# Kernel optimization log

Measured on AMD Instinct MI355X. Metric: run time of the kernel, lower is better.

Reference implementation:

```python
import jax, jax.numpy as jnp
import numpy as np

N = 100000   # nodes
E = 1600000  # edges
F_IN = 64    # n_features
H = 32       # hidden_size
OUT = 1      # output_size


def _lin(k, fan_in, fan_out):
    return (jax.random.normal(k, (fan_in, fan_out), jnp.float32) / np.sqrt(fan_in)).astype(jnp.float32)


def setup_inputs() -> dict:
    key = jax.random.key(0)
    ks = jax.random.split(key, 16)
    x = jax.random.normal(ks[0], (N, F_IN), jnp.float32)
    edge_index = jax.random.randint(ks[1], (2, E), 0, N, dtype=jnp.int64)
    # guarantee current_node (=0) has outgoing edges so the legal-move mask is non-empty
    edge_index = edge_index.at[0, :64].set(0)
    edge_attr = jax.random.uniform(ks[2], (E,), jnp.float32)
    return {
        "x": x, "edge_index": edge_index, "edge_attr": edge_attr, "current_node": 0,
        # conv_in: GraphConv(F_IN -> H)
        "Win_rel": _lin(ks[3], F_IN, H), "bin_rel": jnp.zeros((H,), jnp.float32), "Win_root": _lin(ks[4], F_IN, H),
        # conv_hidden: GraphConv(H -> H)
        "Wh_rel": _lin(ks[5], H, H), "bh_rel": jnp.zeros((H,), jnp.float32), "Wh_root": _lin(ks[6], H, H),
        # policy_conv: GraphConv(H -> OUT)
        "Wp_rel": _lin(ks[7], H, OUT), "bp_rel": jnp.zeros((OUT,), jnp.float32), "Wp_root": _lin(ks[8], H, OUT),
        # value_conv: GraphConv(H -> OUT)
        "Wv_rel": _lin(ks[9], H, OUT), "bv_rel": jnp.zeros((OUT,), jnp.float32), "Wv_root": _lin(ks[10], H, OUT),
    }


def _graph_conv(h, src, dst, ew, W_rel, b_rel, W_root):
    # PyG GraphConv: out_i = W_root h_i + W_rel * sum_{j->i} e_ji * h_j + b
    msg = h[src] * ew[:, None]                              # [E, d] gather + scale
    agg = jax.ops.segment_sum(msg, dst, num_segments=N)      # [N, d] scatter-add
    return agg @ W_rel + b_rel + h @ W_root


def reference(x, edge_index, edge_attr, current_node,
              Win_rel, bin_rel, Win_root,
              Wh_rel, bh_rel, Wh_root,
              Wp_rel, bp_rel, Wp_root,
              Wv_rel, bv_rel, Wv_root):
    src, dst = edge_index[0], edge_index[1]
    h = jax.nn.relu(_graph_conv(x, src, dst, edge_attr, Win_rel, bin_rel, Win_root))
    h = jax.nn.relu(_graph_conv(h, src, dst, edge_attr, Wh_rel, bh_rel, Wh_root))
    p = _graph_conv(h, src, dst, edge_attr, Wp_rel, bp_rel, Wp_root)  # [N, 1]
    v = _graph_conv(h, src, dst, edge_attr, Wv_rel, bv_rel, Wv_root)  # [N, 1]
    # illegal_moves_mask: 1 for nodes directly reachable from current_node
    hit = (src == current_node).astype(jnp.float32)
    mask = (jnp.zeros((N,), jnp.float32).at[dst].add(hit) > 0).astype(jnp.float32)
    p_m = mask * p.T                                   # [1, N]
    p_m = jnp.where(p_m == 0, -jnp.inf, p_m)
    p_soft = jax.nn.softmax(p_m, axis=1)
    v_m = mask * v.T                                   # [1, N]
    return p_soft.reshape(-1), v_m.reshape(-1)
```

## Files before the change

kernel.cpp:

```cpp
#include <hip/hip_runtime.h>
#include <hip/hip_fp16.h>
#include <cmath>

static constexpr int NN = 100000;
static constexpr int NE = 1600000;
static const size_t NW = (size_t)NN * 32;
static constexpr int SUB = 256;
static constexpr int NSUB = 391;
static constexpr int CH = 8192;
static constexpr int NCH = (NE + CH - 1) / CH;
static constexpr int BCAP = 5200;
static constexpr int CSRN = NSUB * BCAP;
static constexpr int MCAP = 4096;

__device__ __forceinline__ float ent_w(unsigned e)
{
    return __half2float(__ushort_as_half((unsigned short)(e >> 17)));
}
__device__ __forceinline__ int ent_s(unsigned e)
{
    int s = (int)(e & 0x1FFFF);
    return s < NN ? s : NN - 1;
}

__device__ __forceinline__ float4 pack8(const float* v)
{
    union { __half2 h2[4]; float4 f4; } u;
    u.h2[0] = __floats2half2_rn(v[0], v[1]);
    u.h2[1] = __floats2half2_rn(v[2], v[3]);
    u.h2[2] = __floats2half2_rn(v[4], v[5]);
    u.h2[3] = __floats2half2_rn(v[6], v[7]);
    return u.f4;
}

__global__ void __launch_bounds__(512) fused_build_mm1_k(
    const int* __restrict__ src, const int* __restrict__ dst,
    const float* __restrict__ ew, const int* __restrict__ curp,
    int* __restrict__ maskb, int* __restrict__ mcount, int* __restrict__ mlist,
    int* __restrict__ bcnt, unsigned* __restrict__ bx,
    unsigned char* __restrict__ bd,
    const float* __restrict__ x, const float* __restrict__ Wrel,
    const float* __restrict__ Wroot, const float* __restrict__ bin,
    __half* __restrict__ proj1, __half* __restrict__ root1)
{
    __shared__ union {
        struct {
            unsigned sBufX[CH];
            unsigned char sBufD[CH];
            int lhist[NSUB];
            int lpos[NSUB];
            int lstart[NSUB];
            int lbase[NSUB];
            int tscan[512];
        } s;
        struct {
            float sX[128 * 65];
            float sW[64 * 68];
        } m;
    } u;

    int t = threadIdx.x;
    int bid = blockIdx.x;

    if (bid < NCH) {
        for (int i = t; i < NSUB; i += 512) { u.s.lhist[i] = 0; u.s.lpos[i] = 0; }
        __syncthreads();
        int c0 = bid * CH;
        int cur = curp[0];
        unsigned rx[CH / 512];
        int rd[CH / 512];
#pragma unroll
        for (int it = 0; it < CH / 512; ++it) {
            int e = c0 + it * 512 + t;
            rd[it] = -1;
            if (e < NE) {
                int d = dst[e];
                int sv = src[e];
                if ((unsigned)d < (unsigned)NN) {
                    rd[it] = d;
                    unsigned bits = __half_as_ushort(__float2half(ew[e]));
                    rx[it] = ((unsigned)sv & 0x1FFFF) | (bits << 17);
                    atomicAdd(&u.s.lhist[d >> 8], 1);
                    if (sv == cur) {
                        if (atomicExch(maskb + d, 1) == 0) {
                            int idx = atomicAdd(mcount, 1);
                            if (idx < MCAP) mlist[idx] = d;
                        }
                    }
                }
            }
        }
        __syncthreads();
        int v = (t < NSUB) ? u.s.lhist[t] : 0;
        u.s.tscan[t] = v;
        __syncthreads();
        for (int sh = 1; sh < 512; sh <<= 1) {
            int xv = u.s.tscan[t];
            int a = (t >= sh) ? u.s.tscan[t - sh] : 0;
            __syncthreads();
            u.s.tscan[t] = xv + a;
            __syncthreads();
        }
        if (t < NSUB) {
            u.s.lstart[t] = u.s.tscan[t] - v;
            u.s.lbase[t] = (v > 0) ? atomicAdd(&bcnt[t], v) : 0;
        }
        __syncthreads();
#pragma unroll
        for (int it = 0; it < CH / 512; ++it) {
            if (rd[it] >= 0) {
                int b = rd[it] >> 8;
                int p = atomicAdd(&u.s.lpos[b], 1);
                int pos = u.s.lstart[b] + p;
                u.s.sBufX[pos] = rx[it];
                u.s.sBufD[pos] = (unsigned char)(rd[it] & 255);
            }
        }
        __syncthreads();
        int grp = t >> 4, l16 = t & 15;
        for (int b = grp; b < NSUB; b += 32) {
            int s0 = u.s.lstart[b];
            int cb = u.s.lhist[b];
            int gb = u.s.lbase[b];
            size_t gb0 = (size_t)b * BCAP;
            for (int j = l16; j < cb; j += 16) {
                unsigned pos = (unsigned)(gb + j);
                if (pos < (unsigned)BCAP) {
                    bx[gb0 + pos] = u.s.sBufX[s0 + j];
                    bd[gb0 + pos] = u.s.sBufD[s0 + j];
                }
            }
        }
    } else {
        int mb = bid - NCH;
        for (int i = t; i < 64 * 32; i += 512) {
            int k = i >> 5, j = i & 31;
            u.m.sW[k * 68 + j] = Wrel[i];
            u.m.sW[k * 68 + 32 + j] = Wroot[i];
        }
        int base = mb * 128;
        for (int i = t; i < 2048; i += 512) {
            int node = i >> 4;
            int k = (i & 15) * 4;
            int n = base + node;
            if (n >= NN) n = NN - 1;
            float4 v4 = *(const float4*)(x + (size_t)n * 64 + k);
            float* p = u.m.sX + node * 65 + k;
            p[0] = v4.x; p[1] = v4.y; p[2] = v4.z; p[3] = v4.w;
        }
        __syncthreads();
        int cg = t & 7;
        int ng = t >> 3;
        int c0m = 8 * cg;
        float acc[2][8] = {};
        for (int k = 0; k < 64; ++k) {
            float xv0 = u.m.sX[(2 * ng + 0) * 65 + k];
            float xv1 = u.m.sX[(2 * ng + 1) * 65 + k];
            float4 w0 = *(const float4*)(u.m.sW + k * 68 + c0m);
            float4 w1 = *(const float4*)(u.m.sW + k * 68 + c0m + 4);
            const float* wp = (const float*)&w0;
#pragma unroll
            for (int j = 0; j < 4; ++j) {
                float w = wp[j];
                acc[0][j] = fmaf(xv0, w, acc[0][j]);
                acc[1][j] = fmaf(xv1, w, acc[1][j]);
            }
            const float* wq = (const float*)&w1;
#pragma unroll
            for (int j = 0; j < 4; ++j) {
                float w = wq[j];
                acc[0][4 + j] = fmaf(xv0, w, acc[0][4 + j]);
                acc[1][4 + j] = fmaf(xv1, w, acc[1][4 + j]);
            }
        }
#pragma unroll
        for (int r = 0; r < 2; ++r) {
            int n = base + 2 * ng + r;
            if (n >= NN) break;
            if (cg < 4) {
                *(float4*)(proj1 + (size_t)n * 32 + c0m) = pack8(acc[r]);
            } else {
                int c = c0m - 32;
                float vv[8];
#pragma unroll
                for (int j = 0; j < 8; ++j) vv[j] = acc[r][j] + bin[c + j];
                *(float4*)(root1 + (size_t)n * 32 + c) = pack8(vv);
            }
        }
    }
}

__global__ void __launch_bounds__(512) sortB_k(
    const unsigned* __restrict__ bx, const unsigned char* __restrict__ bd,
    const int* __restrict__ bcnt,
    unsigned* __restrict__ csr4, int* __restrict__ deg, int* __restrict__ off)
{
    __shared__ unsigned sX[BCAP];
    __shared__ unsigned char sD[BCAP];
    __shared__ int lhist[SUB];
    __shared__ int lstart[SUB];
    __shared__ int lcur[SUB];
    __shared__ int tscan[256];
    int g = blockIdx.x, t = threadIdx.x;
    if (t < SUB) { lhist[t] = 0; lcur[t] = 0; }
    __syncthreads();
    int cnt = bcnt[g];
    if (cnt < 0) cnt = 0;
    if (cnt > BCAP) cnt = BCAP;
    size_t gbase = (size_t)g * BCAP;
    for (int i = t; i < cnt; i += 512) {
        unsigned e = bx[gbase + i];
        unsigned char d = bd[gbase + i];
        sX[i] = e;
        sD[i] = d;
        atomicAdd(&lhist[d], 1);
    }
    __syncthreads();
    if (t < 256) tscan[t] = lhist[t];
    __syncthreads();
    for (int s = 1; s < 256; s <<= 1) {
        int x = 0, a = 0;
        if (t < 256) { x = tscan[t]; a = (t >= s) ? tscan[t - s] : 0; }
        __syncthreads();
        if (t < 256) tscan[t] = x + a;
        __syncthreads();
    }
    if (t < 256) lstart[t] = tscan[t] - lhist[t];
    __syncthreads();
    int base = g * BCAP;
    for (int i = t; i < cnt; i += 512) {
        int ld = (int)sD[i];
        int p = atomicAdd(&lcur[ld], 1);
        unsigned pos = (unsigned)(base + lstart[ld] + p);
        if (pos < (unsigned)CSRN) csr4[pos] = sX[i];
    }
    if (t < SUB) {
        int n = g * SUB + t;
        if (n < NN) {
            deg[n] = lhist[t];
            off[n] = base + lstart[t];
        }
    }
}

__global__ void __launch_bounds__(256) mm2_k(
    const __half* __restrict__ h1, const float* __restrict__ Wrel,
    const float* __restrict__ Wroot, const float* __restrict__ bh,
    __half* __restrict__ proj2, __half* __restrict__ root2)
{
    __shared__ float sX[128 * 33];
    __shared__ float sW[32 * 68];
    int t = threadIdx.x;
    for (int i = t; i < 32 * 32; i += 256) {
        int k = i >> 5, j = i & 31;
        sW[k * 68 + j] = Wrel[i];
        sW[k * 68 + 32 + j] = Wroot[i];
    }
    int base = blockIdx.x * 128;
    for (int i = t; i < 512; i += 256) {
        int node = i >> 2;
        int hs = (i & 3) * 8;
        int n = base + node;
        if (n >= NN) n = NN - 1;
        float4 v = *(const float4*)(h1 + (size_t)n * 32 + hs);
        const __half2* hp = (const __half2*)&v;
        float* p = sX + node * 33 + hs;
#pragma unroll
        for (int u = 0; u < 4; ++u) {
            float2 f2 = __half22float2(hp[u]);
            p[2 * u] = f2.x;
            p[2 * u + 1] = f2.y;
        }
    }
    __syncthreads();
    int cg = t & 7;
    int ng = t >> 3;
    int c0 = 8 * cg;
    float acc[4][8] = {};
    for (int k = 0; k < 32; ++k) {
        float xv0 = sX[(4 * ng + 0) * 33 + k];
        float xv1 = sX[(4 * ng + 1) * 33 + k];
        float xv2 = sX[(4 * ng + 2) * 33 + k];
        float xv3 = sX[(4 * ng + 3) * 33 + k];
        float4 w0 = *(const float4*)(sW + k * 68 + c0);
        float4 w1 = *(const float4*)(sW + k * 68 + c0 + 4);
        const float* wp = (const float*)&w0;
#pragma unroll
        for (int j = 0; j < 4; ++j) {
            float w = wp[j];
            acc[0][j] = fmaf(xv0, w, acc[0][j]);
            acc[1][j] = fmaf(xv1, w, acc[1][j]);
            acc[2][j] = fmaf(xv2, w, acc[2][j]);
            acc[3][j] = fmaf(xv3, w, acc[3][j]);
        }
        const float* wq = (const float*)&w1;
#pragma unroll
        for (int j = 0; j < 4; ++j) {
            float w = wq[j];
            acc[0][4 + j] = fmaf(xv0, w, acc[0][4 + j]);
            acc[1][4 + j] = fmaf(xv1, w, acc[1][4 + j]);
            acc[2][4 + j] = fmaf(xv2, w, acc[2][4 + j]);
            acc[3][4 + j] = fmaf(xv3, w, acc[3][4 + j]);
        }
    }
#pragma unroll
    for (int r = 0; r < 4; ++r) {
        int n = base + 4 * ng + r;
        if (n >= NN) break;
        if (cg < 4) {
            *(float4*)(proj2 + (size_t)n * 32 + c0) = pack8(acc[r]);
        } else {
            int c = c0 - 32;
            float v[8];
#pragma unroll
            for (int j = 0; j < 8; ++j) v[j] = acc[r][j] + bh[c + j];
            *(float4*)(root2 + (size_t)n * 32 + c) = pack8(v);
        }
    }
}

__global__ void __launch_bounds__(256) agg1_v4(
    const __half* __restrict__ proj1, const __half* __restrict__ root1,
    const unsigned* __restrict__ csr4, const int* __restrict__ off,
    const int* __restrict__ deg, __half* __restrict__ h1)
{
    int t = threadIdx.x;
    int q = t & 3;
    int f0 = q * 8;
    int n = blockIdx.x * 64 + (t >> 2);
    if (n >= NN) return;
    int st = off[n];
    int dg = deg[n];
    if (st < 0) st = 0;
    if (st > CSRN) st = CSRN;
    if (dg < 0) dg = 0;
    if (dg > CSRN - st) dg = CSRN - st;
    float acc[8] = {0.f, 0.f, 0.f, 0.f, 0.f, 0.f, 0.f, 0.f};
    int i = 0;
    for (; i + 1 < dg; i += 2) {
        unsigned e0 = csr4[st + i];
        unsigned e1 = csr4[st + i + 1];
        float w0 = ent_w(e0), w1 = ent_w(e1);
        float4 r0 = *(const float4*)(proj1 + (size_t)ent_s(e0) * 32 + f0);
        float4 r1 = *(const float4*)(proj1 + (size_t)ent_s(e1) * 32 + f0);
        const __half2* h0 = (const __half2*)&r0;
        const __half2* h1p = (const __half2*)&r1;
#pragma unroll
        for (int u = 0; u < 4; ++u) {
            float2 a = __half22float2(h0[u]);
            float2 b = __half22float2(h1p[u]);
            acc[2 * u] = fmaf(w0, a.x, acc[2 * u]);
            acc[2 * u + 1] = fmaf(w0, a.y, acc[2 * u + 1]);
            acc[2 * u] = fmaf(w1, b.x, acc[2 * u]);
            acc[2 * u + 1] = fmaf(w1, b.y, acc[2 * u + 1]);
        }
    }
    if (i < dg) {
        unsigned e0 = csr4[st + i];
        float w0 = ent_w(e0);
        float4 r0 = *(const float4*)(proj1 + (size_t)ent_s(e0) * 32 + f0);
        const __half2* h0 = (const __half2*)&r0;
#pragma unroll
        for (int u = 0; u < 4; ++u) {
            float2 a = __half22float2(h0[u]);
            acc[2 * u] = fmaf(w0, a.x, acc[2 * u]);
            acc[2 * u + 1] = fmaf(w0, a.y, acc[2 * u + 1]);
        }
    }
    float4 rr = *(const float4*)(root1 + (size_t)n * 32 + f0);
    const __half2* rp = (const __half2*)&rr;
    float h[8];
#pragma unroll
    for (int u = 0; u < 4; ++u) {
        float2 f2 = __half22float2(rp[u]);
        h[2 * u] = fmaxf(acc[2 * u] + f2.x, 0.f);
        h[2 * u + 1] = fmaxf(acc[2 * u + 1] + f2.y, 0.f);
    }
    *(float4*)(h1 + (size_t)n * 32 + f0) = pack8(h);
}

__global__ void __launch_bounds__(256) agg2_v4(
    const __half* __restrict__ proj2, const __half* __restrict__ root2,
    const float* __restrict__ Wp_rel, const float* __restrict__ Wp_root,
    const float* __restrict__ bp, const float* __restrict__ Wv_rel,
    const float* __restrict__ Wv_root, const float* __restrict__ bv,
    const unsigned* __restrict__ csr4, const int* __restrict__ off,
    const int* __restrict__ deg, float2* __restrict__ pv,
    float* __restrict__ pbase, float* __restrict__ vbase,
    float* __restrict__ out_p, float* __restrict__ out_v)
{
    __shared__ float sHead[4 * 32];
    if (threadIdx.x < 32) {
        sHead[threadIdx.x] = Wp_rel[threadIdx.x];
        sHead[32 + threadIdx.x] = Wp_root[threadIdx.x];
        sHead[64 + threadIdx.x] = Wv_rel[threadIdx.x];
        sHead[96 + threadIdx.x] = Wv_root[threadIdx.x];
    }
    __syncthreads();
    int t = threadIdx.x;
    int q = t & 3;
    int f0 = q * 8;
    int n = blockIdx.x * 64 + (t >> 2);
    if (n >= NN) return;
    int st = off[n];
    int dg = deg[n];
    if (st < 0) st = 0;
    if (st > CSRN) st = CSRN;
    if (dg < 0) dg = 0;
    if (dg > CSRN - st) dg = CSRN - st;
    float acc[8] = {0.f, 0.f, 0.f, 0.f, 0.f, 0.f, 0.f, 0.f};
    int i = 0;
    for (; i + 1 < dg; i += 2) {
        unsigned e0 = csr4[st + i];
        unsigned e1 = csr4[st + i + 1];
        float w0 = ent_w(e0), w1 = ent_w(e1);
        float4 r0 = *(const float4*)(proj2 + (size_t)ent_s(e0) * 32 + f0);
        float4 r1 = *(const float4*)(proj2 + (size_t)ent_s(e1) * 32 + f0);
        const __half2* h0 = (const __half2*)&r0;
        const __half2* h1p = (const __half2*)&r1;
#pragma unroll
        for (int u = 0; u < 4; ++u) {
            float2 a = __half22float2(h0[u]);
            float2 b = __half22float2(h1p[u]);
            acc[2 * u] = fmaf(w0, a.x, acc[2 * u]);
            acc[2 * u + 1] = fmaf(w0, a.y, acc[2 * u + 1]);
            acc[2 * u] = fmaf(w1, b.x, acc[2 * u]);
            acc[2 * u + 1] = fmaf(w1, b.y, acc[2 * u + 1]);
        }
    }
    if (i < dg) {
        unsigned e0 = csr4[st + i];
        float w0 = ent_w(e0);
        float4 r0 = *(const float4*)(proj2 + (size_t)ent_s(e0) * 32 + f0);
        const __half2* h0 = (const __half2*)&r0;
#pragma unroll
        for (int u = 0; u < 4; ++u) {
            float2 a = __half22float2(h0[u]);
            acc[2 * u] = fmaf(w0, a.x, acc[2 * u]);
            acc[2 * u + 1] = fmaf(w0, a.y, acc[2 * u + 1]);
        }
    }
    float4 rr = *(const float4*)(root2 + (size_t)n * 32 + f0);
    const __half2* rp = (const __half2*)&rr;
    float h[8];
#pragma unroll
    for (int u = 0; u < 4; ++u) {
        float2 f2 = __half22float2(rp[u]);
        h[2 * u] = fmaxf(acc[2 * u] + f2.x, 0.f);
        h[2 * u + 1] = fmaxf(acc[2 * u + 1] + f2.y, 0.f);
    }
    float prv = 0.f, pov = 0.f, vrv = 0.f, vov = 0.f;
#pragma unroll
    for (int j = 0; j < 8; ++j) {
        prv = fmaf(h[j], sHead[f0 + j], prv);
        pov = fmaf(h[j], sHead[32 + f0 + j], pov);
        vrv = fmaf(h[j], sHead[64 + f0 + j], vrv);
        vov = fmaf(h[j], sHead[96 + f0 + j], vov);
    }
#pragma unroll
    for (int m = 1; m <= 2; m <<= 1) {
        prv += __shfl_xor(prv, m, 64);
        pov += __shfl_xor(pov, m, 64);
        vrv += __shfl_xor(vrv, m, 64);
        vov += __shfl_xor(vov, m, 64);
    }
    if (q == 0) {
        pv[n] = make_float2(prv, vrv);
        pbase[n] = pov + bp[0];
        vbase[n] = vov + bv[0];
        out_p[n] = 0.f;
        out_v[n] = 0.f;
    }
}

__global__ void __launch_bounds__(256) masked_softmax_k(
    const int* __restrict__ mlist, const int* __restrict__ mcount,
    const unsigned* __restrict__ csr4, const int* __restrict__ off,
    const int* __restrict__ deg, const float2* __restrict__ pv,
    const float* __restrict__ pbase, const float* __restrict__ vbase,
    float* __restrict__ out_p, float* __restrict__ out_v)
{
    __shared__ float sPm[MCAP];
    __shared__ float sV[MCAP];
    __shared__ int sN[MCAP];
    __shared__ float sMx, sSum;
    __shared__ float sred[4];
    int m = mcount[0];
    if (m > MCAP) m = MCAP;
    if (m < 0) m = 0;
    for (int idx = threadIdx.x; idx < m; idx += 256) {
        int n = mlist[idx];
        if ((unsigned)n >= (unsigned)NN) n = 0;
        sN[idx] = n;
        int st = off[n];
        int dg = deg[n];
        if (st < 0) st = 0;
        if (st > CSRN) st = CSRN;
        if (dg < 0) dg = 0;
        if (dg > CSRN - st) dg = CSRN - st;
        float pa = 0.f, va = 0.f;
        for (int i = 0; i < dg; ++i) {
            unsigned ent = csr4[st + i];
            int s = ent_s(ent);
            float w = ent_w(ent);
            float2 tv = pv[s];
            pa = fmaf(tv.x, w, pa);
            va = fmaf(tv.y, w, va);
        }
        float p = pa + pbase[n];
        sPm[idx] = (p == 0.f) ? -INFINITY : p;
        sV[idx] = va + vbase[n];
    }
    __syncthreads();
    float mx = -INFINITY;
    for (int i = threadIdx.x; i < m; i += 256) mx = fmaxf(mx, sPm[i]);
#pragma unroll
    for (int k = 32; k; k >>= 1) mx = fmaxf(mx, __shfl_xor(mx, k, 64));
    if ((threadIdx.x & 63) == 0) sred[threadIdx.x >> 6] = mx;
    __syncthreads();
    if (threadIdx.x == 0)
        sMx = fmaxf(fmaxf(sred[0], sred[1]), fmaxf(sred[2], sred[3]));
    __syncthreads();
    float sum = 0.f;
    for (int i = threadIdx.x; i < m; i += 256) {
        float x = sPm[i];
        sum += (x == -INFINITY) ? 0.f : expf(x - sMx);
    }
#pragma unroll
    for (int k = 32; k; k >>= 1) sum += __shfl_xor(sum, k, 64);
    if ((threadIdx.x & 63) == 0) sred[threadIdx.x >> 6] = sum;
    __syncthreads();
    if (threadIdx.x == 0) sSum = sred[0] + sred[1] + sred[2] + sred[3];
    __syncthreads();
    for (int idx = threadIdx.x; idx < m; idx += 256) {
        int n = sN[idx];
        float x = sPm[idx];
        out_p[n] = (x == -INFINITY) ? 0.f : expf(x - sMx) / sSum;
        out_v[n] = sV[idx];
    }
}

extern "C" void kernel_launch(void* const* d_in, const int* in_sizes, int n_in,
                              void* d_out, int out_size, void* d_ws,
                              size_t ws_size, hipStream_t stream)
{
    const float* x        = (const float*)d_in[0];
    const int*   ei       = (const int*)d_in[1];
    const float* ew       = (const float*)d_in[2];
    const int*   cur      = (const int*)d_in[3];
    const float* Win_rel  = (const float*)d_in[4];
    const float* bin_rel  = (const float*)d_in[5];
    const float* Win_root = (const float*)d_in[6];
    const float* Wh_rel   = (const float*)d_in[7];
    const float* bh_rel   = (const float*)d_in[8];
    const float* Wh_root  = (const float*)d_in[9];
    const float* Wp_rel   = (const float*)d_in[10];
    const float* bp       = (const float*)d_in[11];
    const float* Wp_root  = (const float*)d_in[12];
    const float* Wv_rel   = (const float*)d_in[13];
    const float* bv       = (const float*)d_in[14];
    const float* Wv_root  = (const float*)d_in[15];

    const int* srcA = ei;
    const int* dstA = ei + NE;

    char* w8 = (char*)d_ws;
    unsigned* csr4 = (unsigned*)w8;
    int* deg    = (int*)(csr4 + CSRN);
    int* off    = deg + NN;
    int* maskb  = off + NN;
    int* mcount = maskb + NN;
    int* bcnt   = mcount + 8;
    int* mlist  = bcnt + 400;
    __half* proj1 = (__half*)(mlist + MCAP);
    __half* root1 = proj1 + NW;
    __half* h1    = root1 + NW;
    __half* proj2 = h1 + NW;
    __half* root2 = proj2 + NW;
    float2* pv    = (float2*)(root2 + NW);
    float* pbase  = (float*)(pv + NN);
    float* vbase  = pbase + NN;
    unsigned* bucket_x = (unsigned*)(vbase + NN);
    unsigned char* bucket_d = (unsigned char*)(bucket_x + CSRN);

    float* out_p = (float*)d_out;
    float* out_v = out_p + NN;

    const int NB_MM    = (NN + 127) / 128;
    const int NB_AGG   = (NN + 63) / 64;
    const int NB_FUSED = NCH + NB_MM;

    hipMemsetAsync(maskb, 0, ((size_t)NN + 8 + 400) * sizeof(int), stream);

    fused_build_mm1_k<<<NB_FUSED, 512, 0, stream>>>(
        srcA, dstA, ew, cur, maskb, mcount, mlist, bcnt, bucket_x, bucket_d,
        x, Win_rel, Win_root, bin_rel, proj1, root1);
    sortB_k<<<NSUB, 512, 0, stream>>>(bucket_x, bucket_d, bcnt, csr4, deg, off);

    agg1_v4<<<NB_AGG, 256, 0, stream>>>(proj1, root1, csr4, off, deg, h1);
    mm2_k<<<NB_MM, 256, 0, stream>>>(h1, Wh_rel, Wh_root, bh_rel, proj2, root2);
    agg2_v4<<<NB_AGG, 256, 0, stream>>>(proj2, root2, Wp_rel, Wp_root, bp,
                                        Wv_rel, Wv_root, bv, csr4, off, deg,
                                        pv, pbase, vbase, out_p, out_v);
    masked_softmax_k<<<1, 256, 0, stream>>>(mlist, mcount, csr4, off, deg, pv,
                                            pbase, vbase, out_p, out_v);
}
```

Before: 244.2 us.

## Fuse per-bucket CSR sort with first-layer aggregation in one kernel

Merges the bucket sort kernel and the first aggregation kernel. Each 1024-thread block sorts its 256-node bucket into shared memory, writes the CSR out coalesced, and then aggregates the layer-1 messages straight from shared memory. This saves one launch and the global re-read of the CSR entries, offsets and degrees. The cost is only 391 blocks of 1024 threads with about 47KB of shared memory each, so occupancy and parallelism in the gather-heavy aggregation phase may drop.

```diff
diff --git a/kernel.cpp b/kernel.cpp
--- a/kernel.cpp
+++ b/kernel.cpp
@@ -190,13 +190,16 @@
     }
 }
 
-__global__ void __launch_bounds__(512) sortB_k(
+__global__ void __launch_bounds__(1024) sortagg1_k(
     const unsigned* __restrict__ bx, const unsigned char* __restrict__ bd,
     const int* __restrict__ bcnt,
-    unsigned* __restrict__ csr4, int* __restrict__ deg, int* __restrict__ off)
+    const __half* __restrict__ proj1, const __half* __restrict__ root1,
+    unsigned* __restrict__ csr4, int* __restrict__ deg, int* __restrict__ off,
+    __half* __restrict__ h1)
 {
     __shared__ unsigned sX[BCAP];
     __shared__ unsigned char sD[BCAP];
+    __shared__ unsigned sE[BCAP];
     __shared__ int lhist[SUB];
     __shared__ int lstart[SUB];
     __shared__ int lcur[SUB];
@@ -208,7 +211,7 @@
     if (cnt < 0) cnt = 0;
     if (cnt > BCAP) cnt = BCAP;
     size_t gbase = (size_t)g * BCAP;
-    for (int i = t; i < cnt; i += 512) {
+    for (int i = t; i < cnt; i += 1024) {
         unsigned e = bx[gbase + i];
         unsigned char d = bd[gbase + i];
         sX[i] = e;
@@ -227,13 +230,14 @@
     }
     if (t < 256) lstart[t] = tscan[t] - lhist[t];
     __syncthreads();
-    int base = g * BCAP;
-    for (int i = t; i < cnt; i += 512) {
+    for (int i = t; i < cnt; i += 1024) {
         int ld = (int)sD[i];
         int p = atomicAdd(&lcur[ld], 1);
-        unsigned pos = (unsigned)(base + lstart[ld] + p);
-        if (pos < (unsigned)CSRN) csr4[pos] = sX[i];
-    }
+        int pos = lstart[ld] + p;
+        if ((unsigned)pos < (unsigned)BCAP) sE[pos] = sX[i];
+    }
+    __syncthreads();
+    int base = g * BCAP;
     if (t < SUB) {
         int n = g * SUB + t;
         if (n < NN) {
@@ -241,6 +245,63 @@
             off[n] = base + lstart[t];
         }
     }
+    for (int i = t; i < cnt; i += 1024) {
+        unsigned pos = (unsigned)(base + i);
+        if (pos < (unsigned)CSRN) csr4[pos] = sE[i];
+    }
+    int q = t & 3;
+    int f0 = q * 8;
+    int l = t >> 2;
+    int n = g * SUB + l;
+    if (n >= NN) return;
+    int st = lstart[l];
+    int dg = lhist[l];
+    if (st < 0) st = 0;
+    if (st > BCAP) st = BCAP;
+    if (dg < 0) dg = 0;
+    if (dg > BCAP - st) dg = BCAP - st;
+    float acc[8] = {0.f, 0.f, 0.f, 0.f, 0.f, 0.f, 0.f, 0.f};
+    int i = 0;
+    for (; i + 1 < dg; i += 2) {
+        unsigned e0 = sE[st + i];
+        unsigned e1 = sE[st + i + 1];
+        float w0 = ent_w(e0), w1 = ent_w(e1);
+        float4 r0 = *(const float4*)(proj1 + (size_t)ent_s(e0) * 32 + f0);
+        float4 r1 = *(const float4*)(proj1 + (size_t)ent_s(e1) * 32 + f0);
+        const __half2* h0 = (const __half2*)&r0;
+        const __half2* h1p = (const __half2*)&r1;
+#pragma unroll
+        for (int u = 0; u < 4; ++u) {
+            float2 a = __half22float2(h0[u]);
+            float2 b = __half22float2(h1p[u]);
+            acc[2 * u] = fmaf(w0, a.x, acc[2 * u]);
+            acc[2 * u + 1] = fmaf(w0, a.y, acc[2 * u + 1]);
+            acc[2 * u] = fmaf(w1, b.x, acc[2 * u]);
+            acc[2 * u + 1] = fmaf(w1, b.y, acc[2 * u + 1]);
+        }
+    }
+    if (i < dg) {
+        unsigned e0 = sE[st + i];
+        float w0 = ent_w(e0);
+        float4 r0 = *(const float4*)(proj1 + (size_t)ent_s(e0) * 32 + f0);
+        const __half2* h0 = (const __half2*)&r0;
+#pragma unroll
+        for (int u = 0; u < 4; ++u) {
+            float2 a = __half22float2(h0[u]);
+            acc[2 * u] = fmaf(w0, a.x, acc[2 * u]);
+            acc[2 * u + 1] = fmaf(w0, a.y, acc[2 * u + 1]);
+        }
+    }
+    float4 rr = *(const float4*)(root1 + (size_t)n * 32 + f0);
+    const __half2* rp = (const __half2*)&rr;
+    float h[8];
+#pragma unroll
+    for (int u = 0; u < 4; ++u) {
+        float2 f2 = __half22float2(rp[u]);
+        h[2 * u] = fmaxf(acc[2 * u] + f2.x, 0.f);
+        h[2 * u + 1] = fmaxf(acc[2 * u + 1] + f2.y, 0.f);
+    }
+    *(float4*)(h1 + (size_t)n * 32 + f0) = pack8(h);
 }
 
 __global__ void __launch_bounds__(256) mm2_k(
@@ -317,66 +378,6 @@
             *(float4*)(root2 + (size_t)n * 32 + c) = pack8(v);
         }
     }
-}
-
-__global__ void __launch_bounds__(256) agg1_v4(
-    const __half* __restrict__ proj1, const __half* __restrict__ root1,
-    const unsigned* __restrict__ csr4, const int* __restrict__ off,
-    const int* __restrict__ deg, __half* __restrict__ h1)
-{
-    int t = threadIdx.x;
-    int q = t & 3;
-    int f0 = q * 8;
-    int n = blockIdx.x * 64 + (t >> 2);
-    if (n >= NN) return;
-    int st = off[n];
-    int dg = deg[n];
-    if (st < 0) st = 0;
-    if (st > CSRN) st = CSRN;
-    if (dg < 0) dg = 0;
-    if (dg > CSRN - st) dg = CSRN - st;
-    float acc[8] = {0.f, 0.f, 0.f, 0.f, 0.f, 0.f, 0.f, 0.f};
-    int i = 0;
-    for (; i + 1 < dg; i += 2) {
-        unsigned e0 = csr4[st + i];
-        unsigned e1 = csr4[st + i + 1];
-        float w0 = ent_w(e0), w1 = ent_w(e1);
-        float4 r0 = *(const float4*)(proj1 + (size_t)ent_s(e0) * 32 + f0);
-        float4 r1 = *(const float4*)(proj1 + (size_t)ent_s(e1) * 32 + f0);
-        const __half2* h0 = (const __half2*)&r0;
-        const __half2* h1p = (const __half2*)&r1;
-#pragma unroll
-        for (int u = 0; u < 4; ++u) {
-            float2 a = __half22float2(h0[u]);
-            float2 b = __half22float2(h1p[u]);
-            acc[2 * u] = fmaf(w0, a.x, acc[2 * u]);
-            acc[2 * u + 1] = fmaf(w0, a.y, acc[2 * u + 1]);
-            acc[2 * u] = fmaf(w1, b.x, acc[2 * u]);
-            acc[2 * u + 1] = fmaf(w1, b.y, acc[2 * u + 1]);
-        }
-    }
-    if (i < dg) {
-        unsigned e0 = csr4[st + i];
-        float w0 = ent_w(e0);
-        float4 r0 = *(const float4*)(proj1 + (size_t)ent_s(e0) * 32 + f0);
-        const __half2* h0 = (const __half2*)&r0;
-#pragma unroll
-        for (int u = 0; u < 4; ++u) {
-            float2 a = __half22float2(h0[u]);
-            acc[2 * u] = fmaf(w0, a.x, acc[2 * u]);
-            acc[2 * u + 1] = fmaf(w0, a.y, acc[2 * u + 1]);
-        }
-    }
-    float4 rr = *(const float4*)(root1 + (size_t)n * 32 + f0);
-    const __half2* rp = (const __half2*)&rr;
-    float h[8];
-#pragma unroll
-    for (int u = 0; u < 4; ++u) {
-        float2 f2 = __half22float2(rp[u]);
-        h[2 * u] = fmaxf(acc[2 * u] + f2.x, 0.f);
-        h[2 * u + 1] = fmaxf(acc[2 * u + 1] + f2.y, 0.f);
-    }
-    *(float4*)(h1 + (size_t)n * 32 + f0) = pack8(h);
 }
 
 __global__ void __launch_bounds__(256) agg2_v4(
@@ -595,9 +596,8 @@
     fused_build_mm1_k<<<NB_FUSED, 512, 0, stream>>>(
         srcA, dstA, ew, cur, maskb, mcount, mlist, bcnt, bucket_x, bucket_d,
         x, Win_rel, Win_root, bin_rel, proj1, root1);
-    sortB_k<<<NSUB, 512, 0, stream>>>(bucket_x, bucket_d, bcnt, csr4, deg, off);
-
-    agg1_v4<<<NB_AGG, 256, 0, stream>>>(proj1, root1, csr4, off, deg, h1);
+    sortagg1_k<<<NSUB, 1024, 0, stream>>>(bucket_x, bucket_d, bcnt,
+                                          proj1, root1, csr4, deg, off, h1);
     mm2_k<<<NB_MM, 256, 0, stream>>>(h1, Wh_rel, Wh_root, bh_rel, proj2, root2);
     agg2_v4<<<NB_AGG, 256, 0, stream>>>(proj2, root2, Wp_rel, Wp_root, bp,
                                         Wv_rel, Wv_root, bv, csr4, off, deg,
```

Measured after the change: 229.1 us. 1.07x faster.
